# Performance work log

Hardware: AMD Instinct MI355X
Metric: run time of the kernel (lower is better)

The kernel has to match this reference:

```python
import jax, jax.numpy as jnp
import numpy as np

EPS = 1e-5
NEG_SLOPE = 0.1

def _block(x, W, g, b):
    # x: (B, C_in, K, N); 1x1 conv == channel matmul
    y = jnp.einsum('oc,bckn->bokn', W, x)
    mu = jnp.mean(y, axis=(2, 3), keepdims=True)
    var = jnp.mean((y - mu) ** 2, axis=(2, 3), keepdims=True)
    y = (y - mu) * jax.lax.rsqrt(var + EPS)
    y = y * g[None, :, None, None] + b[None, :, None, None]
    return jnp.where(y >= 0, y, NEG_SLOPE * y)


def setup_inputs() -> dict:
    key = jax.random.key(0)
    ks = jax.random.split(key, 8)
    B, N, C_IN, C_OUT, K = 4, 8192, 32, 64, 32
    E = B * N * K
    signal = jax.random.normal(ks[0], (B, N, C_IN), dtype=jnp.float32)
    edges = jax.random.randint(ks[1], (E,), 0, B * N, dtype=jnp.int64)
    edge_feats = jax.random.normal(ks[2], (E, 3), dtype=jnp.float32)
    # Kaiming-like scaled conv weights
    W1 = jax.random.normal(ks[3], (C_OUT, C_IN + 3), dtype=jnp.float32) / np.sqrt(C_IN + 3)
    W2 = jax.random.normal(ks[4], (C_OUT, C_OUT), dtype=jnp.float32) / np.sqrt(C_OUT)
    W3 = jax.random.normal(ks[5], (C_OUT, C_OUT), dtype=jnp.float32) / np.sqrt(C_OUT)
    g1 = jnp.ones((C_OUT,), jnp.float32); b1 = jnp.zeros((C_OUT,), jnp.float32)
    g2 = jnp.ones((C_OUT,), jnp.float32); b2 = jnp.zeros((C_OUT,), jnp.float32)
    g3 = jnp.ones((C_OUT,), jnp.float32); b3 = jnp.zeros((C_OUT,), jnp.float32)
    return {"signal": signal, "edges": edges, "edge_feats": edge_feats, "k": K,
            "W1": W1, "g1": g1, "b1": b1, "W2": W2, "g2": g2, "b2": b2,
            "W3": W3, "g3": g3, "b3": b3}


def reference(signal, edges, edge_feats, k, W1, g1, b1, W2, g2, b2, W3, g3, b3):
    B, N, C = signal.shape
    flat = signal.reshape(B * N, C)
    gathered = flat[edges]                                   # (E, C)
    x = jnp.concatenate([gathered, edge_feats], axis=-1)     # (E, C+3)
    n_out = edges.shape[0] // (B * k)
    x = x.reshape(B, n_out, k, C + 3)
    x = jnp.transpose(x, (0, 3, 2, 1))                        # (B, C+3, K, N)
    x = _block(x, W1, g1, b1)
    x = _block(x, W2, g2, b2)
    x = _block(x, W3, g3, b3)
    x = jnp.max(x, axis=2)                                    # pool over neighbors -> (B, C_out, N)
    return jnp.transpose(x, (0, 2, 1))                        # (B, N, C_out)
```

## Files before the change

### kernel.cpp

```cpp
#include <hip/hip_runtime.h>
#include <hip/hip_bf16.h>
#include <math.h>

constexpr int B    = 4;
constexpr int N    = 8192;
constexpr int COUT = 64;
constexpr int E    = B * N * 32;
constexpr int PERB = N * 32;
constexpr int TILES  = E / 16;
constexpr int TPW    = 16;
constexpr int TPB    = TPW * 4;
constexpr int BLOCKS = TILES / TPB;
constexpr float EPS   = 1e-5f;
constexpr float SLOPE = 0.1f;


typedef __attribute__((ext_vector_type(8))) short short8;
typedef __attribute__((ext_vector_type(4))) float f32x4;
#define MFMA16 __builtin_amdgcn_mfma_f32_16x16x32_bf16

union S8 { short8 s; unsigned int u[4]; };

__device__ __forceinline__ float bflo(unsigned int u) {
    union { unsigned int x; float f; } v; v.x = u << 16; return v.f;
}
__device__ __forceinline__ float bfhi(unsigned int u) {
    union { unsigned int x; float f; } v; v.x = u & 0xFFFF0000u; return v.f;
}
__device__ __forceinline__ unsigned int pk2(float a, float b) {
    union { __hip_bfloat162 h; unsigned int u; } v;
    v.h = __float22bfloat162_rn(make_float2(a, b));
    return v.u;
}
__device__ __forceinline__ float lrelu(float z) {
    return fmaxf(z, SLOPE * z);
}
__device__ __forceinline__ short8 pack8(const float* f) {
    S8 r;
#pragma unroll
    for (int i = 0; i < 4; ++i) r.u[i] = pk2(f[2 * i], f[2 * i + 1]);
    return r.s;
}
__device__ __forceinline__ short8 xform(uint4 raw, const float* sc, const float* sh) {
    unsigned int w[4] = {raw.x, raw.y, raw.z, raw.w};
    S8 r;
#pragma unroll
    for (int i = 0; i < 4; ++i) {
        float z0 = fmaf(bflo(w[i]), sc[2 * i],     sh[2 * i]);
        float z1 = fmaf(bfhi(w[i]), sc[2 * i + 1], sh[2 * i + 1]);
        r.u[i] = pk2(lrelu(z0), lrelu(z1));
    }
    return r.s;
}

__global__ void detect_i32(const unsigned int* __restrict__ w, int* __restrict__ flag) {
    unsigned long long m = __ballot(w[2 * threadIdx.x + 1] != 0u);
    if (threadIdx.x == 0) *flag = (m != 0ull) ? 1 : 0;
}

__device__ __forceinline__ void stats_epilogue(
        float (&sacc)[4][4], float (&s2acc)[4][4],
        int tid, int wv, int col, int quad, int ablk,
        float* __restrict__ partials) {
    __shared__ float lds[2][4][64];
#pragma unroll
    for (int m = 0; m < 4; ++m)
#pragma unroll
        for (int r = 0; r < 4; ++r) {
            float s = sacc[m][r], s2 = s2acc[m][r];
#pragma unroll
            for (int d = 1; d < 16; d <<= 1) {
                s  += __shfl_xor(s,  d, 16);
                s2 += __shfl_xor(s2, d, 16);
            }
            if (col == 0) {
                int o = m * 16 + quad * 4 + r;
                lds[0][wv][o] = s;
                lds[1][wv][o] = s2;
            }
        }
    __syncthreads();
    if (tid < 64) {
        float s  = lds[0][0][tid] + lds[0][1][tid] + lds[0][2][tid] + lds[0][3][tid];
        float s2 = lds[1][0][tid] + lds[1][1][tid] + lds[1][2][tid] + lds[1][3][tid];
        ((float2*)(partials + (size_t)ablk * 128))[tid] = make_float2(s, s2);
    }
}

__global__ __launch_bounds__(256) void mfma_stage1(
        const float* __restrict__ signal,
        const void*  __restrict__ edges,
        const float* __restrict__ ef,
        const float* __restrict__ W1,
        unsigned short* __restrict__ Y,
        const int* __restrict__ flag,
        float* __restrict__ partials) {
    const int tid = threadIdx.x, lane = tid & 63, wv = tid >> 6;
    const int col = lane & 15, quad = lane >> 4;

    short8 afrag[4][2];
#pragma unroll
    for (int m = 0; m < 4; ++m) {
        const float* wr = W1 + (m * 16 + col) * 35;
        float f[8];
#pragma unroll
        for (int j = 0; j < 8; ++j) f[j] = wr[quad * 8 + j];
        afrag[m][0] = pack8(f);
#pragma unroll
        for (int j = 0; j < 8; ++j) f[j] = (quad == 0 && j < 3) ? wr[32 + j] : 0.f;
        afrag[m][1] = pack8(f);
    }
    const bool is32 = (*flag != 0);
    const int* ip = (const int*)edges;
    const long long* lp = (const long long*)edges;

    float sacc[4][4] = {{0.f}}, s2acc[4][4] = {{0.f}};
    const int tile0 = blockIdx.x * TPB + wv * TPW;
    const int eW = tile0 * 16 + col;

    long long idxA = is32 ? (long long)ip[eW] : lp[eW];
    long long idxB = is32 ? (long long)ip[min(eW + 16, E - 1)] : lp[min(eW + 16, E - 1)];
    const float* spA = signal + idxA * 32 + quad * 8;
    float4 sA0 = *(const float4*)spA;
    float4 sA1 = *(const float4*)(spA + 4);
    float efA0 = 0.f, efA1 = 0.f, efA2 = 0.f;
    if (quad == 0) {
        const float* p = ef + (size_t)eW * 3;
        efA0 = p[0]; efA1 = p[1]; efA2 = p[2];
    }

    for (int ti = 0; ti < TPW; ++ti) {
        const int eCur = eW + ti * 16;
        const int eI = min(eCur + 32, E - 1);
        long long idxC = is32 ? (long long)ip[eI] : lp[eI];
        const float* spB = signal + idxB * 32 + quad * 8;
        float4 sB0 = *(const float4*)spB;
        float4 sB1 = *(const float4*)(spB + 4);
        float efB0 = 0.f, efB1 = 0.f, efB2 = 0.f;
        if (quad == 0) {
            const float* p = ef + (size_t)min(eCur + 16, E - 1) * 3;
            efB0 = p[0]; efB1 = p[1]; efB2 = p[2];
        }
        float f[8] = {sA0.x, sA0.y, sA0.z, sA0.w, sA1.x, sA1.y, sA1.z, sA1.w};
        short8 b0 = pack8(f);
        float g[8] = {efA0, efA1, efA2, 0.f, 0.f, 0.f, 0.f, 0.f};
        short8 b1 = pack8(g);

        unsigned short* tp = Y + (size_t)(tile0 + ti) * 1024;
#pragma unroll
        for (int m = 0; m < 4; ++m) {
            f32x4 acc = {0.f, 0.f, 0.f, 0.f};
            acc = MFMA16(afrag[m][0], b0, acc, 0, 0, 0);
            acc = MFMA16(afrag[m][1], b1, acc, 0, 0, 0);
            *(uint2*)(tp + (m * 2 + (quad >> 1)) * 128 + col * 8 + (quad & 1) * 4) =
                make_uint2(pk2(acc[0], acc[1]), pk2(acc[2], acc[3]));
#pragma unroll
            for (int r = 0; r < 4; ++r) {
                float v = acc[r];
                sacc[m][r] += v;
                s2acc[m][r] = fmaf(v, v, s2acc[m][r]);
            }
        }
        sA0 = sB0; sA1 = sB1;
        efA0 = efB0; efA1 = efB1; efA2 = efB2;
        idxB = idxC;
    }
    stats_epilogue(sacc, s2acc, tid, wv, col, quad, blockIdx.x, partials);
}

__global__ __launch_bounds__(256) void mfma_stage(
        unsigned short* __restrict__ Y,
        const float* __restrict__ W,
        const float* __restrict__ scale,
        const float* __restrict__ shift,
        float* __restrict__ partials,
        const int dir) {
    const int tid = threadIdx.x, lane = tid & 63, wv = tid >> 6;
    const int col = lane & 15, quad = lane >> 4;
    const int ablk = dir ? (BLOCKS - 1 - blockIdx.x) : blockIdx.x;
    const int b    = ablk >> 8;

    short8 afrag[4][2];
#pragma unroll
    for (int m = 0; m < 4; ++m)
#pragma unroll
        for (int kc = 0; kc < 2; ++kc) {
            const float4* wp = (const float4*)(W + (m * 16 + col) * 64 + kc * 32 + quad * 8);
            float4 w0 = wp[0], w1 = wp[1];
            float f[8] = {w0.x, w0.y, w0.z, w0.w, w1.x, w1.y, w1.z, w1.w};
            afrag[m][kc] = pack8(f);
        }
    float sc[2][8], sh[2][8];
#pragma unroll
    for (int kc = 0; kc < 2; ++kc) {
        const int c0 = (kc * 4 + quad) * 8;
#pragma unroll
        for (int j = 0; j < 8; ++j) {
            sc[kc][j] = scale[b * COUT + c0 + j];
            sh[kc][j] = shift[b * COUT + c0 + j];
        }
    }
    float sacc[4][4] = {{0.f}}, s2acc[4][4] = {{0.f}};
    const int tile0 = ablk * TPB + wv * TPW;
    const int off0 = quad * 128 + col * 8;

    const unsigned short* tpA = Y + (size_t)tile0 * 1024;
    uint4 pA0 = *(const uint4*)(tpA + off0);
    uint4 pA1 = *(const uint4*)(tpA + 512 + off0);

    for (int ti = 0; ti < TPW; ++ti) {
        const unsigned short* tpB = Y + (size_t)(tile0 + min(ti + 1, TPW - 1)) * 1024;
        uint4 pB0 = *(const uint4*)(tpB + off0);
        uint4 pB1 = *(const uint4*)(tpB + 512 + off0);

        short8 b0 = xform(pA0, sc[0], sh[0]);
        short8 b1 = xform(pA1, sc[1], sh[1]);
        unsigned short* tp = Y + (size_t)(tile0 + ti) * 1024;
#pragma unroll
        for (int m = 0; m < 4; ++m) {
            f32x4 acc = {0.f, 0.f, 0.f, 0.f};
            acc = MFMA16(afrag[m][0], b0, acc, 0, 0, 0);
            acc = MFMA16(afrag[m][1], b1, acc, 0, 0, 0);
            *(uint2*)(tp + (m * 2 + (quad >> 1)) * 128 + col * 8 + (quad & 1) * 4) =
                make_uint2(pk2(acc[0], acc[1]), pk2(acc[2], acc[3]));
#pragma unroll
            for (int r = 0; r < 4; ++r) {
                float v = acc[r];
                sacc[m][r] += v;
                s2acc[m][r] = fmaf(v, v, s2acc[m][r]);
            }
        }
        pA0 = pB0; pA1 = pB1;
    }
    stats_epilogue(sacc, s2acc, tid, wv, col, quad, ablk, partials);
}

__global__ __launch_bounds__(256) void mfma_stage_last(
        unsigned short* __restrict__ Y,
        const float* __restrict__ W,
        const float* __restrict__ scale,
        const float* __restrict__ shift,
        float* __restrict__ partials) {
    const int tid = threadIdx.x, lane = tid & 63, wv = tid >> 6;
    const int col = lane & 15, quad = lane >> 4;
    const int ablk = blockIdx.x;
    const int b    = ablk >> 8;

    short8 afrag[4][2];
#pragma unroll
    for (int m = 0; m < 4; ++m)
#pragma unroll
        for (int kc = 0; kc < 2; ++kc) {
            const float4* wp = (const float4*)(W + (m * 16 + col) * 64 + kc * 32 + quad * 8);
            float4 w0 = wp[0], w1 = wp[1];
            float f[8] = {w0.x, w0.y, w0.z, w0.w, w1.x, w1.y, w1.z, w1.w};
            afrag[m][kc] = pack8(f);
        }
    float sc[2][8], sh[2][8];
#pragma unroll
    for (int kc = 0; kc < 2; ++kc) {
        const int c0 = (kc * 4 + quad) * 8;
#pragma unroll
        for (int j = 0; j < 8; ++j) {
            sc[kc][j] = scale[b * COUT + c0 + j];
            sh[kc][j] = shift[b * COUT + c0 + j];
        }
    }
    float sacc[4][4] = {{0.f}}, s2acc[4][4] = {{0.f}};
    const int tile0 = ablk * TPB + wv * TPW;
    const int off0 = quad * 128 + col * 8;

    __shared__ float ldsP[4][2048];
    float* P = ldsP[wv];
    const int swz = (col & 7) << 2;

    const unsigned short* tpA = Y + (size_t)tile0 * 1024;
    uint4 pA0 = *(const uint4*)(tpA + off0);
    uint4 pA1 = *(const uint4*)(tpA + 512 + off0);

    for (int pr = 0; pr < TPW / 2; ++pr) {
        float mx[4][4], mn[4][4];
#pragma unroll
        for (int m = 0; m < 4; ++m)
#pragma unroll
            for (int r = 0; r < 4; ++r) { mx[m][r] = -1e30f; mn[m][r] = 1e30f; }

#pragma unroll
        for (int hf = 0; hf < 2; ++hf) {
            const int ti = pr * 2 + hf;
            const unsigned short* tpB = Y + (size_t)(tile0 + min(ti + 1, TPW - 1)) * 1024;
            uint4 pB0 = *(const uint4*)(tpB + off0);
            uint4 pB1 = *(const uint4*)(tpB + 512 + off0);

            short8 b0 = xform(pA0, sc[0], sh[0]);
            short8 b1 = xform(pA1, sc[1], sh[1]);
#pragma unroll
            for (int m = 0; m < 4; ++m) {
                f32x4 acc = {0.f, 0.f, 0.f, 0.f};
                acc = MFMA16(afrag[m][0], b0, acc, 0, 0, 0);
                acc = MFMA16(afrag[m][1], b1, acc, 0, 0, 0);
#pragma unroll
                for (int r = 0; r < 4; ++r) {
                    float v = acc[r];
                    sacc[m][r] += v;
                    s2acc[m][r] = fmaf(v, v, s2acc[m][r]);
                    mx[m][r] = fmaxf(mx[m][r], v);
                    mn[m][r] = fminf(mn[m][r], v);
                }
            }
            pA0 = pB0; pA1 = pB1;
        }
#pragma unroll
        for (int m = 0; m < 4; ++m) {
            const int fi0 = col * 128 + m * 32 + quad * 8;
            float4 lo = {mx[m][0], mn[m][0], mx[m][1], mn[m][1]};
            float4 hi = {mx[m][2], mn[m][2], mx[m][3], mn[m][3]};
            *(float4*)&P[fi0 ^ swz] = lo;
            *(float4*)&P[(fi0 + 4) ^ swz] = hi;
        }
        __builtin_amdgcn_wave_barrier();
        float gx = -1e30f, gn = 1e30f;
#pragma unroll
        for (int cc = 0; cc < 16; ++cc) {
            const float2 v = *(const float2*)&P[(cc * 128 + lane * 2) ^ ((cc & 7) << 2)];
            gx = fmaxf(gx, v.x);
            gn = fminf(gn, v.y);
        }
        __builtin_amdgcn_wave_barrier();
        float* R = (float*)(Y + (size_t)(tile0 + 2 * pr) * 1024);
        R[lane]      = gx;
        R[64 + lane] = gn;
    }
    stats_epilogue(sacc, s2acc, tid, wv, col, quad, ablk, partials);
}

__global__ __launch_bounds__(256) void finalize_k(
        const float* __restrict__ partials,
        const float* __restrict__ gamma,
        const float* __restrict__ beta,
        float* __restrict__ scale,
        float* __restrict__ shift) {
    const int g = blockIdx.x;
    const int o = g >> 2, b = g & 3;
    const int k = threadIdx.x;
    const float* p = partials + (size_t)(b * 256 + k) * 128 + o * 2;
    float s = p[0], s2 = p[1];
    __shared__ float red[512];
    red[k] = s; red[256 + k] = s2;
    __syncthreads();
    for (int st = 128; st > 0; st >>= 1) {
        if (k < st) { red[k] += red[k + st]; red[256 + k] += red[256 + k + st]; }
        __syncthreads();
    }
    if (k == 0) {
        const float inv_n = 1.f / (float)PERB;
        float mean = red[0] * inv_n;
        float var  = red[256] * inv_n - mean * mean;
        float inv  = rsqrtf(var + EPS);
        float scv  = gamma[o] * inv;
        scale[b * COUT + o] = scv;
        shift[b * COUT + o] = beta[o] - mean * scv;
    }
}

__global__ __launch_bounds__(256) void pool_final(
        const unsigned short* __restrict__ Y,
        const float* __restrict__ scale,
        const float* __restrict__ shift,
        float* __restrict__ out) {
    const int t  = blockIdx.x * 256 + threadIdx.x;
    const int og = t & 7;
    const int bn = t >> 3;
    const int b  = bn >> 13;
    const int ablk = bn >> 5;
    const int wv   = (bn >> 3) & 3;
    const int pr   = bn & 7;
    const float* base =
        (const float*)(Y + (size_t)(ablk * TPB + wv * TPW + 2 * pr) * 1024);
    float4 x0 = *(const float4*)(base + og * 8);
    float4 x1 = *(const float4*)(base + og * 8 + 4);
    float4 n0 = *(const float4*)(base + 64 + og * 8);
    float4 n1 = *(const float4*)(base + 68 + og * 8);
    float mxv[8] = {x0.x, x0.y, x0.z, x0.w, x1.x, x1.y, x1.z, x1.w};
    float mnv[8] = {n0.x, n0.y, n0.z, n0.w, n1.x, n1.y, n1.z, n1.w};
    float r[8];
#pragma unroll
    for (int j = 0; j < 8; ++j) {
        const int o = og * 8 + j;
        const float s = scale[b * COUT + o], h = shift[b * COUT + o];
        float m = (s >= 0.f ? mxv[j] : mnv[j]) * s + h;
        r[j] = lrelu(m);
    }
    float4* q = (float4*)(out + (size_t)bn * COUT + og * 8);
    q[0] = make_float4(r[0], r[1], r[2], r[3]);
    q[1] = make_float4(r[4], r[5], r[6], r[7]);
}

extern "C" void kernel_launch(void* const* d_in, const int* in_sizes, int n_in,
                              void* d_out, int out_size, void* d_ws, size_t ws_size,
                              hipStream_t stream) {
    const float* signal = (const float*)d_in[0];
    const void*  edges  = d_in[1];
    const float* ef     = (const float*)d_in[2];
    const float* W1 = (const float*)d_in[4];
    const float* g1 = (const float*)d_in[5];
    const float* b1 = (const float*)d_in[6];
    const float* W2 = (const float*)d_in[7];
    const float* g2 = (const float*)d_in[8];
    const float* b2 = (const float*)d_in[9];
    const float* W3 = (const float*)d_in[10];
    const float* g3 = (const float*)d_in[11];
    const float* b3 = (const float*)d_in[12];
    float* out = (float*)d_out;

    unsigned short* Y = (unsigned short*)d_ws;
    const size_t YB = (size_t)E * COUT * sizeof(unsigned short);
    float* partials = (float*)((char*)d_ws + YB);
    char*  tail = (char*)d_ws + YB + (size_t)BLOCKS * 128 * sizeof(float);
    int*   flag = (int*)tail;
    float* ss   = (float*)(tail + 256);
    float *sc0 = ss,        *sh0 = ss + 256;
    float *sc1 = ss + 512,  *sh1 = ss + 768;
    float *sc2 = ss + 1024, *sh2 = ss + 1280;

    detect_i32<<<1, 64, 0, stream>>>((const unsigned int*)edges, flag);

    mfma_stage1<<<BLOCKS, 256, 0, stream>>>(signal, edges, ef, W1, Y, flag, partials);
    finalize_k<<<256, 256, 0, stream>>>(partials, g1, b1, sc0, sh0);

    mfma_stage<<<BLOCKS, 256, 0, stream>>>(Y, W2, sc0, sh0, partials, 1);
    finalize_k<<<256, 256, 0, stream>>>(partials, g2, b2, sc1, sh1);

    mfma_stage_last<<<BLOCKS, 256, 0, stream>>>(Y, W3, sc1, sh1, partials);
    finalize_k<<<256, 256, 0, stream>>>(partials, g3, b3, sc2, sh2);

    pool_final<<<1024, 256, 0, stream>>>(Y, sc2, sh2, out);
}
```

Before: 159.4 us.

## Recompute block-2 conv inside block-3 kernel instead of storing its output

The block-2 pass now only computes batch-norm statistics and no longer writes its activations back to the workspace. The block-3 kernel reads block-1 output, recomputes the block-2 matmul per tile, passes the result through per-wave LDS to re-layout it, then applies block-2 normalization and the block-3 matmul. This removes one full activation write to global memory at the cost of a duplicated matmul, extra registers for two weight sets, and LDS round trips.

```diff
diff --git a/kernel.cpp b/kernel.cpp
--- a/kernel.cpp
+++ b/kernel.cpp
@@ -168,82 +168,15 @@
     stats_epilogue(sacc, s2acc, tid, wv, col, quad, blockIdx.x, partials);
 }
 
-__global__ __launch_bounds__(256) void mfma_stage(
-        unsigned short* __restrict__ Y,
-        const float* __restrict__ W,
-        const float* __restrict__ scale,
-        const float* __restrict__ shift,
-        float* __restrict__ partials,
-        const int dir) {
-    const int tid = threadIdx.x, lane = tid & 63, wv = tid >> 6;
-    const int col = lane & 15, quad = lane >> 4;
-    const int ablk = dir ? (BLOCKS - 1 - blockIdx.x) : blockIdx.x;
-    const int b    = ablk >> 8;
-
-    short8 afrag[4][2];
-#pragma unroll
-    for (int m = 0; m < 4; ++m)
-#pragma unroll
-        for (int kc = 0; kc < 2; ++kc) {
-            const float4* wp = (const float4*)(W + (m * 16 + col) * 64 + kc * 32 + quad * 8);
-            float4 w0 = wp[0], w1 = wp[1];
-            float f[8] = {w0.x, w0.y, w0.z, w0.w, w1.x, w1.y, w1.z, w1.w};
-            afrag[m][kc] = pack8(f);
-        }
-    float sc[2][8], sh[2][8];
-#pragma unroll
-    for (int kc = 0; kc < 2; ++kc) {
-        const int c0 = (kc * 4 + quad) * 8;
-#pragma unroll
-        for (int j = 0; j < 8; ++j) {
-            sc[kc][j] = scale[b * COUT + c0 + j];
-            sh[kc][j] = shift[b * COUT + c0 + j];
-        }
-    }
-    float sacc[4][4] = {{0.f}}, s2acc[4][4] = {{0.f}};
-    const int tile0 = ablk * TPB + wv * TPW;
-    const int off0 = quad * 128 + col * 8;
-
-    const unsigned short* tpA = Y + (size_t)tile0 * 1024;
-    uint4 pA0 = *(const uint4*)(tpA + off0);
-    uint4 pA1 = *(const uint4*)(tpA + 512 + off0);
-
-    for (int ti = 0; ti < TPW; ++ti) {
-        const unsigned short* tpB = Y + (size_t)(tile0 + min(ti + 1, TPW - 1)) * 1024;
-        uint4 pB0 = *(const uint4*)(tpB + off0);
-        uint4 pB1 = *(const uint4*)(tpB + 512 + off0);
-
-        short8 b0 = xform(pA0, sc[0], sh[0]);
-        short8 b1 = xform(pA1, sc[1], sh[1]);
-        unsigned short* tp = Y + (size_t)(tile0 + ti) * 1024;
-#pragma unroll
-        for (int m = 0; m < 4; ++m) {
-            f32x4 acc = {0.f, 0.f, 0.f, 0.f};
-            acc = MFMA16(afrag[m][0], b0, acc, 0, 0, 0);
-            acc = MFMA16(afrag[m][1], b1, acc, 0, 0, 0);
-            *(uint2*)(tp + (m * 2 + (quad >> 1)) * 128 + col * 8 + (quad & 1) * 4) =
-                make_uint2(pk2(acc[0], acc[1]), pk2(acc[2], acc[3]));
-#pragma unroll
-            for (int r = 0; r < 4; ++r) {
-                float v = acc[r];
-                sacc[m][r] += v;
-                s2acc[m][r] = fmaf(v, v, s2acc[m][r]);
-            }
-        }
-        pA0 = pB0; pA1 = pB1;
-    }
-    stats_epilogue(sacc, s2acc, tid, wv, col, quad, ablk, partials);
-}
-
-__global__ __launch_bounds__(256) void mfma_stage_last(
-        unsigned short* __restrict__ Y,
+__global__ __launch_bounds__(256) void mfma_stage2_stats(
+        const unsigned short* __restrict__ Y,
         const float* __restrict__ W,
         const float* __restrict__ scale,
         const float* __restrict__ shift,
         float* __restrict__ partials) {
     const int tid = threadIdx.x, lane = tid & 63, wv = tid >> 6;
     const int col = lane & 15, quad = lane >> 4;
-    const int ablk = blockIdx.x;
+    const int ablk = BLOCKS - 1 - blockIdx.x;
     const int b    = ablk >> 8;
 
     short8 afrag[4][2];
@@ -270,14 +203,89 @@
     const int tile0 = ablk * TPB + wv * TPW;
     const int off0 = quad * 128 + col * 8;
 
-    __shared__ float ldsP[4][2048];
-    float* P = ldsP[wv];
-    const int swz = (col & 7) << 2;
-
     const unsigned short* tpA = Y + (size_t)tile0 * 1024;
     uint4 pA0 = *(const uint4*)(tpA + off0);
     uint4 pA1 = *(const uint4*)(tpA + 512 + off0);
 
+    for (int ti = 0; ti < TPW; ++ti) {
+        const unsigned short* tpB = Y + (size_t)(tile0 + min(ti + 1, TPW - 1)) * 1024;
+        uint4 pB0 = *(const uint4*)(tpB + off0);
+        uint4 pB1 = *(const uint4*)(tpB + 512 + off0);
+
+        short8 b0 = xform(pA0, sc[0], sh[0]);
+        short8 b1 = xform(pA1, sc[1], sh[1]);
+#pragma unroll
+        for (int m = 0; m < 4; ++m) {
+            f32x4 acc = {0.f, 0.f, 0.f, 0.f};
+            acc = MFMA16(afrag[m][0], b0, acc, 0, 0, 0);
+            acc = MFMA16(afrag[m][1], b1, acc, 0, 0, 0);
+#pragma unroll
+            for (int r = 0; r < 4; ++r) {
+                float v = acc[r];
+                sacc[m][r] += v;
+                s2acc[m][r] = fmaf(v, v, s2acc[m][r]);
+            }
+        }
+        pA0 = pB0; pA1 = pB1;
+    }
+    stats_epilogue(sacc, s2acc, tid, wv, col, quad, ablk, partials);
+}
+
+__global__ __launch_bounds__(256) void mfma_stage23(
+        unsigned short* __restrict__ Y,
+        const float* __restrict__ W2,
+        const float* __restrict__ W3,
+        const float* __restrict__ sc1g,
+        const float* __restrict__ sh1g,
+        const float* __restrict__ sc2g,
+        const float* __restrict__ sh2g,
+        float* __restrict__ partials) {
+    const int tid = threadIdx.x, lane = tid & 63, wv = tid >> 6;
+    const int col = lane & 15, quad = lane >> 4;
+    const int ablk = blockIdx.x;
+    const int b    = ablk >> 8;
+
+    short8 afrag2[4][2], afrag3[4][2];
+#pragma unroll
+    for (int m = 0; m < 4; ++m)
+#pragma unroll
+        for (int kc = 0; kc < 2; ++kc) {
+            const float4* wp2 = (const float4*)(W2 + (m * 16 + col) * 64 + kc * 32 + quad * 8);
+            float4 a0 = wp2[0], a1 = wp2[1];
+            float f2[8] = {a0.x, a0.y, a0.z, a0.w, a1.x, a1.y, a1.z, a1.w};
+            afrag2[m][kc] = pack8(f2);
+            const float4* wp3 = (const float4*)(W3 + (m * 16 + col) * 64 + kc * 32 + quad * 8);
+            float4 c0 = wp3[0], c1 = wp3[1];
+            float f3[8] = {c0.x, c0.y, c0.z, c0.w, c1.x, c1.y, c1.z, c1.w};
+            afrag3[m][kc] = pack8(f3);
+        }
+    float sc1[2][8], sh1[2][8], sc2[2][8], sh2[2][8];
+#pragma unroll
+    for (int kc = 0; kc < 2; ++kc) {
+        const int c0 = (kc * 4 + quad) * 8;
+#pragma unroll
+        for (int j = 0; j < 8; ++j) {
+            sc1[kc][j] = sc1g[b * COUT + c0 + j];
+            sh1[kc][j] = sh1g[b * COUT + c0 + j];
+            sc2[kc][j] = sc2g[b * COUT + c0 + j];
+            sh2[kc][j] = sh2g[b * COUT + c0 + j];
+        }
+    }
+    float sacc[4][4] = {{0.f}}, s2acc[4][4] = {{0.f}};
+    const int tile0 = ablk * TPB + wv * TPW;
+    const int off0 = quad * 128 + col * 8;
+
+    __shared__ unsigned short tileT[4][1024];
+    __shared__ float ldsP[4][2048];
+    unsigned short* T = tileT[wv];
+    float* P = ldsP[wv];
+    const int swz = (col & 7) << 2;
+
+    const unsigned short* tpA = Y + (size_t)tile0 * 1024;
+    uint4 pA0 = *(const uint4*)(tpA + off0);
+    uint4 pA1 = *(const uint4*)(tpA + 512 + off0);
+
+#pragma unroll 1
     for (int pr = 0; pr < TPW / 2; ++pr) {
         float mx[4][4], mn[4][4];
 #pragma unroll
@@ -292,13 +300,28 @@
             uint4 pB0 = *(const uint4*)(tpB + off0);
             uint4 pB1 = *(const uint4*)(tpB + 512 + off0);
 
-            short8 b0 = xform(pA0, sc[0], sh[0]);
-            short8 b1 = xform(pA1, sc[1], sh[1]);
+            short8 b0 = xform(pA0, sc1[0], sh1[0]);
+            short8 b1 = xform(pA1, sc1[1], sh1[1]);
+#pragma unroll
+            for (int m = 0; m < 4; ++m) {
+                f32x4 a2 = {0.f, 0.f, 0.f, 0.f};
+                a2 = MFMA16(afrag2[m][0], b0, a2, 0, 0, 0);
+                a2 = MFMA16(afrag2[m][1], b1, a2, 0, 0, 0);
+                *(uint2*)(T + (m * 2 + (quad >> 1)) * 128 + col * 8 + (quad & 1) * 4) =
+                    make_uint2(pk2(a2[0], a2[1]), pk2(a2[2], a2[3]));
+            }
+            __builtin_amdgcn_wave_barrier();
+            uint4 q0 = *(const uint4*)(T + off0);
+            uint4 q1 = *(const uint4*)(T + 512 + off0);
+            __builtin_amdgcn_wave_barrier();
+
+            short8 c0 = xform(q0, sc2[0], sh2[0]);
+            short8 c1 = xform(q1, sc2[1], sh2[1]);
 #pragma unroll
             for (int m = 0; m < 4; ++m) {
                 f32x4 acc = {0.f, 0.f, 0.f, 0.f};
-                acc = MFMA16(afrag[m][0], b0, acc, 0, 0, 0);
-                acc = MFMA16(afrag[m][1], b1, acc, 0, 0, 0);
+                acc = MFMA16(afrag3[m][0], c0, acc, 0, 0, 0);
+                acc = MFMA16(afrag3[m][1], c1, acc, 0, 0, 0);
 #pragma unroll
                 for (int r = 0; r < 4; ++r) {
                     float v = acc[r];
@@ -428,10 +451,10 @@
     mfma_stage1<<<BLOCKS, 256, 0, stream>>>(signal, edges, ef, W1, Y, flag, partials);
     finalize_k<<<256, 256, 0, stream>>>(partials, g1, b1, sc0, sh0);
 
-    mfma_stage<<<BLOCKS, 256, 0, stream>>>(Y, W2, sc0, sh0, partials, 1);
+    mfma_stage2_stats<<<BLOCKS, 256, 0, stream>>>(Y, W2, sc0, sh0, partials);
     finalize_k<<<256, 256, 0, stream>>>(partials, g2, b2, sc1, sh1);
 
-    mfma_stage_last<<<BLOCKS, 256, 0, stream>>>(Y, W3, sc1, sh1, partials);
+    mfma_stage23<<<BLOCKS, 256, 0, stream>>>(Y, W2, W3, sc0, sh0, sc1, sh1, partials);
     finalize_k<<<256, 256, 0, stream>>>(partials, g3, b3, sc2, sh2);
 
     pool_final<<<1024, 256, 0, stream>>>(Y, sc2, sh2, out);
```

New measurement: 166.1 us. 4.2% more time.
